# Performance work log

Hardware: AMD Instinct MI355X
Metric: run time of the kernel (lower is better)

The kernel has to match this reference:

```python
import jax, jax.numpy as jnp
import numpy as np

N_USERS, N_ITEMS, N_TOPICS = 200000, 100000, 100
N_NODES = N_USERS + N_ITEMS + N_TOPICS
N_EDGES = 5000000
DIM = 64
LAYERS = 3
BATCH = 16384


def setup_inputs() -> dict:
    key = jax.random.key(0)
    ks = jax.random.split(key, 8)
    users = jax.random.randint(ks[0], (BATCH,), 0, N_USERS, dtype=jnp.int64 if jax.config.jax_enable_x64 else jnp.int32)
    items = jax.random.randint(ks[1], (BATCH,), 0, N_ITEMS, dtype=jnp.int64 if jax.config.jax_enable_x64 else jnp.int32)
    edge_rows = jax.random.randint(ks[2], (N_EDGES,), 0, N_NODES, dtype=jnp.int32)
    edge_cols = jax.random.randint(ks[3], (N_EDGES,), 0, N_NODES, dtype=jnp.int32)
    # values ~ 1/deg to mimic the symmetric-normalized A_hat of LightGCN
    edge_vals = jax.random.uniform(ks[4], (N_EDGES,), dtype=jnp.float32) / 16.0
    user_emb = 0.1 * jax.random.normal(ks[5], (N_USERS, DIM), dtype=jnp.float32)
    item_emb = 0.1 * jax.random.normal(ks[6], (N_ITEMS, DIM), dtype=jnp.float32)
    topic_emb = 0.1 * jax.random.normal(ks[7], (N_TOPICS, DIM), dtype=jnp.float32)
    return {"users": users, "items": items, "edge_rows": edge_rows,
            "edge_cols": edge_cols, "edge_vals": edge_vals,
            "user_emb": user_emb, "item_emb": item_emb, "topic_emb": topic_emb}


def reference(users, items, edge_rows, edge_cols, edge_vals, user_emb, item_emb, topic_emb):
    n_users = user_emb.shape[0]
    n_nodes = n_users + item_emb.shape[0] + topic_emb.shape[0]
    # E^0 = [users; items; topics]
    h = jnp.concatenate([user_emb, item_emb, topic_emb], axis=0)  # [N, dim]
    acc = h
    for _ in range(LAYERS):
        # sparse A_hat @ h : gather source rows, scale by edge weight, scatter-add to dst
        msgs = edge_vals[:, None] * h[edge_cols]                  # [E, dim]
        h = jax.ops.segment_sum(msgs, edge_rows, num_segments=n_nodes)
        acc = acc + h
    out = acc / (LAYERS + 1)                                      # stack-mean over layers
    u = out[users]                                                # [B, dim]
    it = out[n_users + items]                                     # items offset into node table
    return jnp.sum(u * it, axis=1)                                # [B]
```

## Files before the change

kernel.cpp:

```cpp
#include <hip/hip_runtime.h>
#include <hip/hip_fp16.h>

#define N_USERS  200000
#define N_ITEMS  100000
#define N_TOPICS 100
#define N_NODES  (N_USERS + N_ITEMS + N_TOPICS)
#define DIM      64
#define BSHIFT   9
#define BROWS    (1 << BSHIFT)
#define NBUCKETS ((N_NODES + BROWS - 1) >> BSHIFT)
#define COLMASK  0x7FFFF
#define NB       512
#define NBSHIFT  9
#define M_TOT    (NBUCKETS * NB)
#define SB       256
#define CH       ((M_TOT + SB - 1) / SB)


__global__ void bucket_hist_kernel(const int* __restrict__ rows,
                                   int* __restrict__ partial, int n_edges) {
    __shared__ int h[NBUCKETS];
    for (int i = threadIdx.x; i < NBUCKETS; i += blockDim.x) h[i] = 0;
    __syncthreads();
    int stride = gridDim.x * blockDim.x;
    for (int e = blockIdx.x * blockDim.x + threadIdx.x; e < n_edges; e += stride)
        atomicAdd(&h[((unsigned)rows[e]) >> BSHIFT], 1);
    __syncthreads();
    for (int i = threadIdx.x; i < NBUCKETS; i += blockDim.x)
        partial[blockIdx.x * NBUCKETS + i] = h[i];
}

__device__ __forceinline__ int phys_idx(int L) {
    return (L & (NB - 1)) * NBUCKETS + (L >> NBSHIFT);
}

__global__ void scanB1_kernel(const int* __restrict__ partial,
                              int* __restrict__ psum) {
    __shared__ int s[256];
    int tid = threadIdx.x;
    int c0 = blockIdx.x * CH;
    int c1 = min(M_TOT, c0 + CH);
    int sum = 0;
    for (int L = c0 + tid; L < c1; L += 256) sum += partial[phys_idx(L)];
    s[tid] = sum;
    __syncthreads();
    for (int off = 128; off > 0; off >>= 1) {
        if (tid < off) s[tid] += s[tid + off];
        __syncthreads();
    }
    if (tid == 0) psum[blockIdx.x] = s[0];
}

__global__ void scanB3_kernel(const int* __restrict__ partial,
                              const int* __restrict__ psum,
                              int* __restrict__ offs) {
    __shared__ int s[SB];
    __shared__ int tile[256];
    __shared__ int carry;
    int tid = threadIdx.x;
    s[tid] = (tid < blockIdx.x) ? psum[tid] : 0;
    __syncthreads();
    for (int off = 128; off > 0; off >>= 1) {
        if (tid < off) s[tid] += s[tid + off];
        __syncthreads();
    }
    if (tid == 0) carry = s[0];
    __syncthreads();
    int c0 = blockIdx.x * CH;
    int c1 = min(M_TOT, c0 + CH);
    for (int base = c0; base < c1; base += 256) {
        int L = base + tid;
        int v = (L < c1) ? partial[phys_idx(L)] : 0;
        tile[tid] = v;
        __syncthreads();
        for (int off = 1; off < 256; off <<= 1) {
            int t = (tid >= off) ? tile[tid - off] : 0;
            __syncthreads();
            tile[tid] += t;
            __syncthreads();
        }
        if (L < c1) offs[L] = carry + tile[tid] - v;
        __syncthreads();
        if (tid == 255) carry += tile[255];
        __syncthreads();
    }
}

__global__ void scatter1_kernel(const int* __restrict__ rows,
                                const int* __restrict__ cols,
                                const float* __restrict__ vals,
                                const int* __restrict__ offs,
                                int2* __restrict__ bkt_buf, int n_edges) {
    __shared__ int lpos[NBUCKETS];
    for (int i = threadIdx.x; i < NBUCKETS; i += blockDim.x)
        lpos[i] = offs[i * NB + blockIdx.x];
    __syncthreads();
    int stride = gridDim.x * blockDim.x;
    for (int e = blockIdx.x * blockDim.x + threadIdx.x; e < n_edges; e += stride) {
        int r = rows[e];
        int b = ((unsigned)r) >> BSHIFT;
        int pos = atomicAdd(&lpos[b], 1);
        int2 p;
        p.x = cols[e] | ((r & (BROWS - 1)) << 19);
        p.y = __float_as_int(vals[e]);
        bkt_buf[pos] = p;
    }
}

__global__ void scatter2_kernel(const int2* __restrict__ bkt_buf,
                                const int* __restrict__ offs,
                                int* __restrict__ row_ptr,
                                int2* __restrict__ csr_cv, int n_edges) {
    __shared__ int lcnt[BROWS];
    __shared__ int lptr[BROWS];
    __shared__ int lfill[BROWS];
    __shared__ int s[256];
    int b = blockIdx.x;
    int t = threadIdx.x;
    int e0 = offs[b * NB];
    int e1 = (b == NBUCKETS - 1) ? n_edges : offs[(b + 1) * NB];
    lcnt[t] = 0;
    lfill[t] = 0;
    __syncthreads();
    for (int e = e0 + t; e < e1; e += blockDim.x)
        atomicAdd(&lcnt[((unsigned)bkt_buf[e].x) >> 19], 1);
    __syncthreads();
    if (t < 256) s[t] = lcnt[2 * t] + lcnt[2 * t + 1];
    __syncthreads();
    for (int off = 1; off < 256; off <<= 1) {
        int v = 0;
        if (t < 256 && t >= off) v = s[t - off];
        __syncthreads();
        if (t < 256) s[t] += v;
        __syncthreads();
    }
    if (t < 256) {
        int base = e0 + (t ? s[t - 1] : 0);
        int rbase = b << BSHIFT;
        int p_even = base;
        int p_odd  = base + lcnt[2 * t];
        lptr[2 * t]     = p_even;
        lptr[2 * t + 1] = p_odd;
        if (rbase + 2 * t     < N_NODES) row_ptr[rbase + 2 * t]     = p_even;
        if (rbase + 2 * t + 1 < N_NODES) row_ptr[rbase + 2 * t + 1] = p_odd;
    }
    if (b == NBUCKETS - 1 && t == 0) row_ptr[N_NODES] = n_edges;
    __syncthreads();
    for (int e = e0 + t; e < e1; e += blockDim.x) {
        int2 p = bkt_buf[e];
        int delta = ((unsigned)p.x) >> 19;
        int pos = lptr[delta] + atomicAdd(&lfill[delta], 1);
        int2 cv;
        cv.x = p.x & COLMASK;
        cv.y = p.y;
        csr_cv[pos] = cv;
    }
}

__global__ void concat_f16_kernel(const float* __restrict__ uemb,
                                  const float* __restrict__ iemb,
                                  const float* __restrict__ temb,
                                  ushort* __restrict__ h0) {
    int g = blockIdx.x * blockDim.x + threadIdx.x;
    long base = (long)g * 4;
    if (base >= (long)N_NODES * DIM) return;
    const float* src;
    long off;
    if (base < (long)N_USERS * DIM)                 { src = uemb; off = base; }
    else if (base < (long)(N_USERS + N_ITEMS) * DIM){ src = iemb; off = base - (long)N_USERS * DIM; }
    else                                            { src = temb; off = base - (long)(N_USERS + N_ITEMS) * DIM; }
    float4 v = *(const float4*)(src + off);
    __half2 a = __floats2half2_rn(v.x, v.y);
    __half2 b = __floats2half2_rn(v.z, v.w);
    uint2 o;
    o.x = *(unsigned*)&a;
    o.y = *(unsigned*)&b;
    ((uint2*)h0)[g] = o;
}

__device__ __forceinline__ float4 fma_mix4(const ushort* __restrict__ h,
                                           int row, int l16, float w,
                                           float4 acc) {
    uint2 r = ((const uint2*)(h + (size_t)row * DIM))[l16];
    __half2 h01 = *(__half2*)&r.x;
    __half2 h23 = *(__half2*)&r.y;
    acc.x = __builtin_fmaf(__half2float(__low2half(h01)),  w, acc.x);
    acc.y = __builtin_fmaf(__half2float(__high2half(h01)), w, acc.y);
    acc.z = __builtin_fmaf(__half2float(__low2half(h23)),  w, acc.z);
    acc.w = __builtin_fmaf(__half2float(__high2half(h23)), w, acc.w);
    return acc;
}

__global__ void spmv_csr_kernel(const int* __restrict__ row_ptr,
                                const int2* __restrict__ csr_cv,
                                const ushort* __restrict__ h_src,
                                ushort* __restrict__ h_dst) {
    int wave = (int)(((long)blockIdx.x * blockDim.x + threadIdx.x) >> 6);
    int lane = threadIdx.x & 63;
    int g    = lane >> 4;
    int l16  = lane & 15;
    int r    = wave * 4 + g;
    int rc   = min(r, N_NODES - 1);
    int p0   = row_ptr[rc];
    int p1   = row_ptr[rc + 1];
    int len  = (r < N_NODES) ? (p1 - p0) : 0;
    int m = max(len, __shfl_xor(len, 16, 64));
    m = max(m, __shfl_xor(m, 32, 64));
    float4 acc = make_float4(0.f, 0.f, 0.f, 0.f);
    for (int off = 0; off < m; off += 8) {
        int2 cv[8];
        #pragma unroll
        for (int j = 0; j < 8; ++j) {
            bool k = (off + j) < len;
            cv[j] = csr_cv[k ? (p0 + off + j) : p0];
            if (!k) cv[j].y = 0;
        }
        #pragma unroll
        for (int j = 0; j < 8; ++j)
            acc = fma_mix4(h_src, cv[j].x, l16, __int_as_float(cv[j].y), acc);
    }
    if (r < N_NODES) {
        __half2 a = __floats2half2_rn(acc.x, acc.y);
        __half2 b = __floats2half2_rn(acc.z, acc.w);
        uint2 o;
        o.x = *(unsigned*)&a;
        o.y = *(unsigned*)&b;
        ((uint2*)(h_dst + (size_t)r * DIM))[l16] = o;
    }
}

__global__ void spmv_batch_kernel(const int* __restrict__ row_ptr,
                                  const int2* __restrict__ csr_cv,
                                  const ushort* __restrict__ h_src,
                                  const int* __restrict__ users,
                                  const int* __restrict__ items,
                                  float* __restrict__ u_acc,
                                  float* __restrict__ it_acc, int B) {
    int wave = (int)(((long)blockIdx.x * blockDim.x + threadIdx.x) >> 6);
    int lane = threadIdx.x & 63;
    int g    = lane >> 4;
    int l16  = lane & 15;
    int s    = wave * 4 + g;
    bool ok  = s < 2 * B;
    int node = 0;
    if (ok) node = (s < B) ? users[s] : (N_USERS + items[s - B]);
    int p0  = row_ptr[node];
    int p1  = row_ptr[node + 1];
    int len = ok ? (p1 - p0) : 0;
    int m = max(len, __shfl_xor(len, 16, 64));
    m = max(m, __shfl_xor(m, 32, 64));
    float4 acc = make_float4(0.f, 0.f, 0.f, 0.f);
    for (int off = 0; off < m; off += 8) {
        int2 cv[8];
        #pragma unroll
        for (int j = 0; j < 8; ++j) {
            bool k = (off + j) < len;
            cv[j] = csr_cv[k ? (p0 + off + j) : p0];
            if (!k) cv[j].y = 0;
        }
        #pragma unroll
        for (int j = 0; j < 8; ++j)
            acc = fma_mix4(h_src, cv[j].x, l16, __int_as_float(cv[j].y), acc);
    }
    if (ok) {
        float* dst = (s < B) ? (u_acc + (size_t)s * DIM)
                             : (it_acc + (size_t)(s - B) * DIM);
        float4* p = (float4*)dst + l16;
        float4 old = *p;
        old.x += acc.x; old.y += acc.y; old.z += acc.z; old.w += acc.w;
        *p = old;
    }
}


__global__ void gather_add_kernel(const ushort* __restrict__ h,
                                  const int* __restrict__ users,
                                  const int* __restrict__ items,
                                  float* __restrict__ u_acc,
                                  float* __restrict__ it_acc,
                                  int B, int first) {
    int gid  = blockIdx.x * blockDim.x + threadIdx.x;
    int b    = gid >> 4;
    int lane = gid & 15;
    if (b >= B) return;
    int u  = users[b];
    int it = N_USERS + items[b];
    uint2 ur = ((const uint2*)(h + (size_t)u  * DIM))[lane];
    uint2 ir = ((const uint2*)(h + (size_t)it * DIM))[lane];
    float2 u01 = __half22float2(*(__half2*)&ur.x);
    float2 u23 = __half22float2(*(__half2*)&ur.y);
    float2 i01 = __half22float2(*(__half2*)&ir.x);
    float2 i23 = __half22float2(*(__half2*)&ir.y);
    float4* up = (float4*)(u_acc  + (size_t)b * DIM) + lane;
    float4* ip = (float4*)(it_acc + (size_t)b * DIM) + lane;
    if (first) {
        *up = make_float4(u01.x, u01.y, u23.x, u23.y);
        *ip = make_float4(i01.x, i01.y, i23.x, i23.y);
    } else {
        float4 a = *up;
        a.x += u01.x; a.y += u01.y; a.z += u23.x; a.w += u23.y;
        *up = a;
        float4 c = *ip;
        c.x += i01.x; c.y += i01.y; c.z += i23.x; c.w += i23.y;
        *ip = c;
    }
}

__global__ void dot_kernel(const float* __restrict__ u_acc,
                           const float* __restrict__ it_acc,
                           float* __restrict__ out, int B) {
    int gid  = blockIdx.x * blockDim.x + threadIdx.x;
    int b    = gid >> 6;
    int lane = gid & 63;
    if (b >= B) return;
    float p = u_acc[(size_t)b * DIM + lane] * it_acc[(size_t)b * DIM + lane];
    #pragma unroll
    for (int off = 32; off > 0; off >>= 1)
        p += __shfl_down(p, off, 64);
    if (lane == 0) out[b] = p * (1.0f / 16.0f);
}

extern "C" void kernel_launch(void* const* d_in, const int* in_sizes, int n_in,
                              void* d_out, int out_size, void* d_ws, size_t ws_size,
                              hipStream_t stream) {
    const int*   users = (const int*)d_in[0];
    const int*   items = (const int*)d_in[1];
    const int*   erows = (const int*)d_in[2];
    const int*   ecols = (const int*)d_in[3];
    const float* evals = (const float*)d_in[4];
    const float* uemb  = (const float*)d_in[5];
    const float* iemb  = (const float*)d_in[6];
    const float* temb  = (const float*)d_in[7];
    float* out = (float*)d_out;

    const int n_edges = in_sizes[2];
    const int B       = in_sizes[0];

    const size_t h2bytes = (((size_t)N_NODES * DIM * 2 + 255) / 256) * 256;
    const size_t abytes  = (size_t)B * DIM * sizeof(float);
    const size_t rpbytes = (((size_t)(N_NODES + 1) * 4 + 255) / 256) * 256;
    const size_t cvbytes = (size_t)n_edges * 8;
    const size_t mbytes  = (((size_t)M_TOT * 4 + 255) / 256) * 256;

    char* ws = (char*)d_ws;
    size_t off = 0;
    ushort* hA      = (ushort*)(ws + off); off += h2bytes;
    ushort* hB      = (ushort*)(ws + off); off += h2bytes;
    float*  u_acc   = (float*) (ws + off); off += abytes;
    float*  it_acc  = (float*) (ws + off); off += abytes;
    int*    row_ptr = (int*)   (ws + off); off += rpbytes;
    int2*   csr_cv  = (int2*)  (ws + off); off += cvbytes;
    int2*   bkt_buf = (int2*)  (ws + off); off += cvbytes;
    int*    partial = (int*)   (ws + off); off += mbytes;
    int*    offs    = (int*)   (ws + off); off += mbytes;
    int*    psum    = (int*)   (ws + off); off += 4096;

    dim3 blk(256);
    dim3 blk512(512);

    bucket_hist_kernel<<<NB, blk512, 0, stream>>>(erows, partial, n_edges);
    scanB1_kernel<<<SB, blk, 0, stream>>>(partial, psum);
    scanB3_kernel<<<SB, blk, 0, stream>>>(partial, psum, offs);
    scatter1_kernel<<<NB, blk512, 0, stream>>>(erows, ecols, evals, offs, bkt_buf, n_edges);
    scatter2_kernel<<<NBUCKETS, blk512, 0, stream>>>(bkt_buf, offs, row_ptr, csr_cv, n_edges);

    const long n4 = (long)N_NODES * DIM / 4;
    concat_f16_kernel<<<(int)((n4 + 255) / 256), blk, 0, stream>>>(uemb, iemb, temb, hA);

    const int gblocks = (B * 16 + 255) / 256;
    gather_add_kernel<<<gblocks, blk, 0, stream>>>(hA, users, items, u_acc, it_acc, B, 1);

    const int nwaves  = (N_NODES + 3) / 4;
    const int sblocks = (int)(((long)nwaves * 64 + 255) / 256);
    ushort* src = hA;
    ushort* dst = hB;
    for (int l = 0; l < 2; ++l) {
        spmv_csr_kernel<<<sblocks, blk, 0, stream>>>(row_ptr, csr_cv, src, dst);
        gather_add_kernel<<<gblocks, blk, 0, stream>>>(dst, users, items, u_acc, it_acc, B, 0);
        ushort* t = src; src = dst; dst = t;
    }
    const int bwaves  = (2 * B + 3) / 4;
    const int bblocks = (int)(((long)bwaves * 64 + 255) / 256);
    spmv_batch_kernel<<<bblocks, blk, 0, stream>>>(row_ptr, csr_cv, src,
                                                   users, items, u_acc, it_acc, B);

    dot_kernel<<<(B * 64 + 255) / 256, blk, 0, stream>>>(u_acc, it_acc, out, B);
}
```

Measured before the change: 591.1 us.

## Replace two-pass bucketed CSR build with direct global-atomic counting sort

Replaces the two-level bucketed radix build (per-block bucket histograms, bucket scatter, then per-bucket local sort) with a direct per-row global-atomic histogram, a row-level scan, and a single scatter that claims slots with global atomics. This drops the intermediate bucket buffer pass and one full read/write of the edge array. In exchange it relies on contended global atomics over 300K rows and writes scattered to random CSR positions, and the edge order within a row becomes nondeterministic.

```diff
diff --git a/kernel.cpp b/kernel.cpp
--- a/kernel.cpp
+++ b/kernel.cpp
@@ -6,42 +6,25 @@
 #define N_TOPICS 100
 #define N_NODES  (N_USERS + N_ITEMS + N_TOPICS)
 #define DIM      64
-#define BSHIFT   9
-#define BROWS    (1 << BSHIFT)
-#define NBUCKETS ((N_NODES + BROWS - 1) >> BSHIFT)
-#define COLMASK  0x7FFFF
-#define NB       512
-#define NBSHIFT  9
-#define M_TOT    (NBUCKETS * NB)
 #define SB       256
-#define CH       ((M_TOT + SB - 1) / SB)
-
-
-__global__ void bucket_hist_kernel(const int* __restrict__ rows,
-                                   int* __restrict__ partial, int n_edges) {
-    __shared__ int h[NBUCKETS];
-    for (int i = threadIdx.x; i < NBUCKETS; i += blockDim.x) h[i] = 0;
-    __syncthreads();
+#define RCH      ((N_NODES + SB - 1) / SB)
+
+
+__global__ void hist_kernel(const int* __restrict__ rows,
+                            int* __restrict__ cnt, int n_edges) {
     int stride = gridDim.x * blockDim.x;
     for (int e = blockIdx.x * blockDim.x + threadIdx.x; e < n_edges; e += stride)
-        atomicAdd(&h[((unsigned)rows[e]) >> BSHIFT], 1);
-    __syncthreads();
-    for (int i = threadIdx.x; i < NBUCKETS; i += blockDim.x)
-        partial[blockIdx.x * NBUCKETS + i] = h[i];
-}
-
-__device__ __forceinline__ int phys_idx(int L) {
-    return (L & (NB - 1)) * NBUCKETS + (L >> NBSHIFT);
-}
-
-__global__ void scanB1_kernel(const int* __restrict__ partial,
+        atomicAdd(&cnt[rows[e]], 1);
+}
+
+__global__ void scanR1_kernel(const int* __restrict__ cnt,
                               int* __restrict__ psum) {
     __shared__ int s[256];
     int tid = threadIdx.x;
-    int c0 = blockIdx.x * CH;
-    int c1 = min(M_TOT, c0 + CH);
+    int c0 = blockIdx.x * RCH;
+    int c1 = min(N_NODES, c0 + RCH);
     int sum = 0;
-    for (int L = c0 + tid; L < c1; L += 256) sum += partial[phys_idx(L)];
+    for (int i = c0 + tid; i < c1; i += 256) sum += cnt[i];
     s[tid] = sum;
     __syncthreads();
     for (int off = 128; off > 0; off >>= 1) {
@@ -51,9 +34,10 @@
     if (tid == 0) psum[blockIdx.x] = s[0];
 }
 
-__global__ void scanB3_kernel(const int* __restrict__ partial,
+__global__ void scanR2_kernel(const int* __restrict__ cnt,
                               const int* __restrict__ psum,
-                              int* __restrict__ offs) {
+                              int* __restrict__ row_ptr,
+                              int* __restrict__ row_next, int n_edges) {
     __shared__ int s[SB];
     __shared__ int tile[256];
     __shared__ int carry;
@@ -66,11 +50,11 @@
     }
     if (tid == 0) carry = s[0];
     __syncthreads();
-    int c0 = blockIdx.x * CH;
-    int c1 = min(M_TOT, c0 + CH);
+    int c0 = blockIdx.x * RCH;
+    int c1 = min(N_NODES, c0 + RCH);
     for (int base = c0; base < c1; base += 256) {
-        int L = base + tid;
-        int v = (L < c1) ? partial[phys_idx(L)] : 0;
+        int i = base + tid;
+        int v = (i < c1) ? cnt[i] : 0;
         tile[tid] = v;
         __syncthreads();
         for (int off = 1; off < 256; off <<= 1) {
@@ -79,80 +63,30 @@
             tile[tid] += t;
             __syncthreads();
         }
-        if (L < c1) offs[L] = carry + tile[tid] - v;
+        if (i < c1) {
+            int ex = carry + tile[tid] - v;
+            row_ptr[i]  = ex;
+            row_next[i] = ex;
+        }
         __syncthreads();
         if (tid == 255) carry += tile[255];
         __syncthreads();
     }
-}
-
-__global__ void scatter1_kernel(const int* __restrict__ rows,
-                                const int* __restrict__ cols,
-                                const float* __restrict__ vals,
-                                const int* __restrict__ offs,
-                                int2* __restrict__ bkt_buf, int n_edges) {
-    __shared__ int lpos[NBUCKETS];
-    for (int i = threadIdx.x; i < NBUCKETS; i += blockDim.x)
-        lpos[i] = offs[i * NB + blockIdx.x];
-    __syncthreads();
+    if (blockIdx.x == gridDim.x - 1 && tid == 0) row_ptr[N_NODES] = n_edges;
+}
+
+__global__ void scatter_csr_kernel(const int* __restrict__ rows,
+                                   const int* __restrict__ cols,
+                                   const float* __restrict__ vals,
+                                   int* __restrict__ row_next,
+                                   int2* __restrict__ csr_cv, int n_edges) {
     int stride = gridDim.x * blockDim.x;
     for (int e = blockIdx.x * blockDim.x + threadIdx.x; e < n_edges; e += stride) {
         int r = rows[e];
-        int b = ((unsigned)r) >> BSHIFT;
-        int pos = atomicAdd(&lpos[b], 1);
-        int2 p;
-        p.x = cols[e] | ((r & (BROWS - 1)) << 19);
-        p.y = __float_as_int(vals[e]);
-        bkt_buf[pos] = p;
-    }
-}
-
-__global__ void scatter2_kernel(const int2* __restrict__ bkt_buf,
-                                const int* __restrict__ offs,
-                                int* __restrict__ row_ptr,
-                                int2* __restrict__ csr_cv, int n_edges) {
-    __shared__ int lcnt[BROWS];
-    __shared__ int lptr[BROWS];
-    __shared__ int lfill[BROWS];
-    __shared__ int s[256];
-    int b = blockIdx.x;
-    int t = threadIdx.x;
-    int e0 = offs[b * NB];
-    int e1 = (b == NBUCKETS - 1) ? n_edges : offs[(b + 1) * NB];
-    lcnt[t] = 0;
-    lfill[t] = 0;
-    __syncthreads();
-    for (int e = e0 + t; e < e1; e += blockDim.x)
-        atomicAdd(&lcnt[((unsigned)bkt_buf[e].x) >> 19], 1);
-    __syncthreads();
-    if (t < 256) s[t] = lcnt[2 * t] + lcnt[2 * t + 1];
-    __syncthreads();
-    for (int off = 1; off < 256; off <<= 1) {
-        int v = 0;
-        if (t < 256 && t >= off) v = s[t - off];
-        __syncthreads();
-        if (t < 256) s[t] += v;
-        __syncthreads();
-    }
-    if (t < 256) {
-        int base = e0 + (t ? s[t - 1] : 0);
-        int rbase = b << BSHIFT;
-        int p_even = base;
-        int p_odd  = base + lcnt[2 * t];
-        lptr[2 * t]     = p_even;
-        lptr[2 * t + 1] = p_odd;
-        if (rbase + 2 * t     < N_NODES) row_ptr[rbase + 2 * t]     = p_even;
-        if (rbase + 2 * t + 1 < N_NODES) row_ptr[rbase + 2 * t + 1] = p_odd;
-    }
-    if (b == NBUCKETS - 1 && t == 0) row_ptr[N_NODES] = n_edges;
-    __syncthreads();
-    for (int e = e0 + t; e < e1; e += blockDim.x) {
-        int2 p = bkt_buf[e];
-        int delta = ((unsigned)p.x) >> 19;
-        int pos = lptr[delta] + atomicAdd(&lfill[delta], 1);
+        int pos = atomicAdd(&row_next[r], 1);
         int2 cv;
-        cv.x = p.x & COLMASK;
-        cv.y = p.y;
+        cv.x = cols[e];
+        cv.y = __float_as_int(vals[e]);
         csr_cv[pos] = cv;
     }
 }
@@ -340,29 +274,28 @@
     const size_t abytes  = (size_t)B * DIM * sizeof(float);
     const size_t rpbytes = (((size_t)(N_NODES + 1) * 4 + 255) / 256) * 256;
     const size_t cvbytes = (size_t)n_edges * 8;
-    const size_t mbytes  = (((size_t)M_TOT * 4 + 255) / 256) * 256;
+    const size_t cbytes  = (((size_t)N_NODES * 4 + 255) / 256) * 256;
 
     char* ws = (char*)d_ws;
     size_t off = 0;
-    ushort* hA      = (ushort*)(ws + off); off += h2bytes;
-    ushort* hB      = (ushort*)(ws + off); off += h2bytes;
-    float*  u_acc   = (float*) (ws + off); off += abytes;
-    float*  it_acc  = (float*) (ws + off); off += abytes;
-    int*    row_ptr = (int*)   (ws + off); off += rpbytes;
-    int2*   csr_cv  = (int2*)  (ws + off); off += cvbytes;
-    int2*   bkt_buf = (int2*)  (ws + off); off += cvbytes;
-    int*    partial = (int*)   (ws + off); off += mbytes;
-    int*    offs    = (int*)   (ws + off); off += mbytes;
-    int*    psum    = (int*)   (ws + off); off += 4096;
+    ushort* hA       = (ushort*)(ws + off); off += h2bytes;
+    ushort* hB       = (ushort*)(ws + off); off += h2bytes;
+    float*  u_acc    = (float*) (ws + off); off += abytes;
+    float*  it_acc   = (float*) (ws + off); off += abytes;
+    int*    row_ptr  = (int*)   (ws + off); off += rpbytes;
+    int2*   csr_cv   = (int2*)  (ws + off); off += cvbytes;
+    int*    row_cnt  = (int*)   (ws + off); off += cbytes;
+    int*    row_next = (int*)   (ws + off); off += cbytes;
+    int*    psum     = (int*)   (ws + off); off += 4096;
 
     dim3 blk(256);
-    dim3 blk512(512);
-
-    bucket_hist_kernel<<<NB, blk512, 0, stream>>>(erows, partial, n_edges);
-    scanB1_kernel<<<SB, blk, 0, stream>>>(partial, psum);
-    scanB3_kernel<<<SB, blk, 0, stream>>>(partial, psum, offs);
-    scatter1_kernel<<<NB, blk512, 0, stream>>>(erows, ecols, evals, offs, bkt_buf, n_edges);
-    scatter2_kernel<<<NBUCKETS, blk512, 0, stream>>>(bkt_buf, offs, row_ptr, csr_cv, n_edges);
+
+    hipMemsetAsync(row_cnt, 0, (size_t)N_NODES * 4, stream);
+    hist_kernel<<<2048, blk, 0, stream>>>(erows, row_cnt, n_edges);
+    scanR1_kernel<<<SB, blk, 0, stream>>>(row_cnt, psum);
+    scanR2_kernel<<<SB, blk, 0, stream>>>(row_cnt, psum, row_ptr, row_next, n_edges);
+    scatter_csr_kernel<<<2048, blk, 0, stream>>>(erows, ecols, evals,
+                                                 row_next, csr_cv, n_edges);
 
     const long n4 = (long)N_NODES * DIM / 4;
     concat_f16_kernel<<<(int)((n4 + 255) / 256), blk, 0, stream>>>(uemb, iemb, temb, hA);
```

Measured after the change: 856.0 us. 44.8% more time.
